# Kernel tuning notes

Hardware: AMD Instinct MI355X
Metric: run time of the kernel (lower is better)

The kernel has to match this reference:

```python
import jax, jax.numpy as jnp
import numpy as np

L = 8        # path length (number of visited nodes)
N = 32768    # neighbors per node (fixed fan-out)
H = 404      # relation_dim == GRU hidden size
D = 128      # node_encode_dim
F = 532      # neighbor feature = D + H
SCALE = 0.05


def setup_inputs() -> dict:
    key = jax.random.key(0)
    ks = jax.random.split(key, 14)
    return {
        "query": jax.random.normal(ks[0], (1, H), jnp.float32),
        "path_nodes": jax.random.normal(ks[1], (L, D), jnp.float32),
        "neighbors": jax.random.normal(ks[2], (L, N, F), jnp.float32),
        "action_ids": jax.random.randint(ks[3], (L - 1,), 0, N),
        "W_ih": jax.random.normal(ks[4], (3 * H, 3 * D), jnp.float32) * SCALE,
        "W_hh": jax.random.normal(ks[5], (3 * H, H), jnp.float32) * SCALE,
        "b_ih": jax.random.normal(ks[6], (3 * H,), jnp.float32) * SCALE,
        "b_hh": jax.random.normal(ks[7], (3 * H,), jnp.float32) * SCALE,
        "W_fa": jax.random.normal(ks[8], (D, F), jnp.float32) * SCALE,
        "b_fa": jax.random.normal(ks[9], (D,), jnp.float32) * SCALE,
        "W_fs": jax.random.normal(ks[10], (D, H), jnp.float32) * SCALE,
        "b_fs": jax.random.normal(ks[11], (D,), jnp.float32) * SCALE,
        "W_fp": jax.random.normal(ks[12], (1, 2 * D), jnp.float32) * SCALE,
        "b_fp": jax.random.normal(ks[13], (1,), jnp.float32) * SCALE,
    }


def gru_cell(x, h, W_ih, W_hh, b_ih, b_hh):
    # torch.nn.GRUCell semantics; x: (1, 3D), h: (1, H)
    gi = x @ W_ih.T + b_ih   # (1, 3H)
    gh = h @ W_hh.T + b_hh   # (1, 3H)
    i_r, i_z, i_n = jnp.split(gi, 3, axis=-1)
    h_r, h_z, h_n = jnp.split(gh, 3, axis=-1)
    r = jax.nn.sigmoid(i_r + h_r)
    z = jax.nn.sigmoid(i_z + h_z)
    n = jnp.tanh(i_n + r * h_n)
    return (1.0 - z) * n + z * h


def reference(query, path_nodes, neighbors, action_ids,
              W_ih, W_hh, b_ih, b_hh, W_fa, b_fa, W_fs, b_fs, W_fp, b_fp):
    # FA over all hops' neighbor blocks at once: (L, N, F) x (D, F) -> (L, N, D)
    hnts = jnp.einsum('lnf,df->lnd', neighbors, W_fa) + b_fa
    hmax = jnp.max(hnts, axis=1)                        # (L, D)  column-wise max (== _Max)
    hsel = hnts[jnp.arange(L - 1), action_ids]          # (L-1, D) chosen-action rows

    # initial GRU step: cat(zeros, zeros, first node emb) with query as hidden
    x0 = jnp.concatenate([jnp.zeros((1, 2 * D), query.dtype), path_nodes[0:1]], axis=1)
    qt = gru_cell(x0, query, W_ih, W_hh, b_ih, b_hh)

    def step(qt, inp):
        hAt, hat, nxt = inp                             # each (D,)
        x = jnp.concatenate([hAt, hat, nxt])[None, :]   # (1, 3D)
        return gru_cell(x, qt, W_ih, W_hh, b_ih, b_hh), None

    qt, _ = jax.lax.scan(step, qt, (hmax[:-1], hsel, path_nodes[1:]))

    hSt = qt @ W_fs.T + b_fs                            # (1, D)
    u0 = jnp.concatenate([hSt, hmax[-1:]], axis=1) @ W_fp.T + b_fp   # (1, 1)
    uks = hSt @ hnts[-1].T                              # (1, N)
    return jax.nn.softmax(jnp.concatenate([u0, uks], axis=1), axis=1)
```

## Files before the change

### kernel.cpp

```cpp
#include <hip/hip_runtime.h>
#include <math.h>

#define L 8
#define N 32768
#define H 404
#define D 128
#define F 532
#define KT 9
#define GRU_BLOCKS 101

typedef __attribute__((ext_vector_type(8))) _Float16 half8;
typedef __attribute__((ext_vector_type(4))) float f32x4;
typedef __attribute__((address_space(3))) unsigned int as3_u32;
typedef __attribute__((address_space(1))) unsigned int as1_u32;

#define WS_WH2     0
#define WS_HMAXK   (WS_WH2 + 36864)
#define WS_HSEL    (WS_HMAXK + L * D)
#define WS_GI      (WS_HSEL + (L - 1) * D)
#define WS_HBUF    (WS_GI + L * 3 * H)
#define WS_V       (WS_HBUF + 2 * H)
#define WS_HS      (WS_V + F)
#define WS_SCAL    (WS_HS + D)
#define WS_CNT     (WS_SCAL + 4)
#define WS_LOGITS  (WS_CNT + 4)

__device__ __forceinline__ unsigned encf(float f) {
    unsigned u = __float_as_uint(f);
    return (u & 0x80000000u) ? ~u : (u | 0x80000000u);
}
__device__ __forceinline__ float decf(unsigned u) {
    unsigned b = (u & 0x80000000u) ? (u ^ 0x80000000u) : ~u;
    return __uint_as_float(b);
}
__device__ __forceinline__ float sigmoidf_(float x) {
    return 1.0f / (1.0f + __expf(-x));
}
__device__ __forceinline__ unsigned pk_f16(float a, float b) {
    auto h = __builtin_amdgcn_cvt_pkrtz(a, b);
    return *(unsigned*)&h;
}
__device__ __forceinline__ half8 pack8(float4 x0, float4 x1) {
    uint4 u = { pk_f16(x0.x, x0.y), pk_f16(x0.z, x0.w),
                pk_f16(x1.x, x1.y), pk_f16(x1.z, x1.w) };
    return *(half8*)&u;
}
__device__ __forceinline__ void gld16(const void* g, void* l) {
    __builtin_amdgcn_global_load_lds((const as1_u32*)g, (as3_u32*)l, 16, 0, 0);
}

__global__ void k_prep(const float* __restrict__ Wfa, unsigned short* __restrict__ wh2,
                       unsigned* __restrict__ keys, unsigned* __restrict__ cnt) {
    int i = blockIdx.x * 256 + threadIdx.x;
    if (i < L * D) keys[i] = 0u;
    if (i == 2000) *cnt = 0u;
    if (i >= KT * 128 * 8) return;
    int kt = i / (128 * 8);
    int rem = i - kt * 128 * 8;
    int c = rem >> 3, j = rem & 7;
    int k0 = kt * 64 + (j ^ (c & 7)) * 8;
    unsigned short v[8];
#pragma unroll
    for (int e = 0; e < 8; ++e) {
        int k = k0 + e;
        float x = (k < F) ? Wfa[c * F + k] : 0.0f;
        _Float16 h = (_Float16)x;
        v[e] = *(unsigned short*)&h;
    }
    *(uint4*)(wh2 + (long)i * 8) = *(uint4*)v;
}

__global__ __launch_bounds__(256, 3)
void k_big(const float* __restrict__ nb, const unsigned short* __restrict__ wh2,
           const float* __restrict__ bfa, const int* __restrict__ aid,
           unsigned* __restrict__ hmaxk, float* __restrict__ hsel) {
    __shared__ float As[128 * 64];
    __shared__ unsigned short Bs[128 * 64];

    const int bid = blockIdx.x;
    const int l_hop = bid >> 8;
    const int row0 = (bid & 255) * 128;
    const int tid = threadIdx.x;
    const int lane = tid & 63, w = tid >> 6;
    const int wm = w >> 1, wn = w & 1;
    const int lr = lane & 15, kg = lane >> 4;

    const float* xbase = nb + ((long)l_hop * N + row0) * F;

    f32x4 acc[4][4];
    float bv[4];
#pragma unroll
    for (int n = 0; n < 4; ++n) bv[n] = bfa[wn * 64 + n * 16 + lr];
#pragma unroll
    for (int m = 0; m < 4; ++m)
#pragma unroll
        for (int n = 0; n < 4; ++n) {
            acc[m][n][0] = bv[n]; acc[m][n][1] = bv[n];
            acc[m][n][2] = bv[n]; acc[m][n][3] = bv[n];
        }

    const int srow = lane >> 4;
    const int scp  = lane & 15;

    for (int kt = 0; kt < KT; ++kt) {
        const int fc = kt * 64;
        __syncthreads();

#pragma unroll
        for (int it = 0; it < 8; ++it) {
            int rbase = it * 16 + w * 4;
            int row = rbase + srow;
            int cg = scp ^ (row & 7);
            int col0 = fc + cg * 4;
            const float* src = xbase + (long)row * F + ((col0 < F) ? col0 : 0);
            gld16(src, (char*)As + rbase * 256);
        }
#pragma unroll
        for (int it = 0; it < 4; ++it) {
            int rb = it * 32 + w * 8;
            const char* src = (const char*)wh2 + (long)kt * 16384 + rb * 128 + lane * 16;
            gld16(src, (char*)Bs + rb * 128);
        }
        __syncthreads();

#pragma unroll
        for (int ks = 0; ks < 2; ++ks) {
            half8 b[4];
#pragma unroll
            for (int n = 0; n < 4; ++n) {
                int col = wn * 64 + n * 16 + lr;
                int ch = (ks * 4 + kg) ^ (col & 7);
                b[n] = *(const half8*)((const char*)Bs + col * 128 + ch * 16);
            }
#pragma unroll
            for (int m = 0; m < 4; ++m) {
                int row = wm * 64 + m * 16 + lr;
                int c0 = ks * 8 + kg * 2;
                const char* base = (const char*)As + row * 256;
                float4 x0 = *(const float4*)(base + (((c0)     ^ (row & 7)) << 4));
                float4 x1 = *(const float4*)(base + (((c0 + 1) ^ (row & 7)) << 4));
                half8 a = pack8(x0, x1);
#pragma unroll
                for (int n = 0; n < 4; ++n)
                    acc[m][n] = __builtin_amdgcn_mfma_f32_16x16x32_f16(a, b[n], acc[m][n], 0, 0, 0);
            }
        }
    }

    __syncthreads();

    if (l_hop < L - 1) {
        int br = aid[l_hop] - row0;
        if (br >= 0 && br < 128 && (br >> 6) == wm && ((br >> 2) & 3) == kg) {
            int msel = (br >> 4) & 3, rsel = br & 3;
#pragma unroll
            for (int n = 0; n < 4; ++n) {
                float vsel = 0.f;
#pragma unroll
                for (int m = 0; m < 4; ++m)
#pragma unroll
                    for (int r = 0; r < 4; ++r)
                        if (m == msel && r == rsel) vsel = acc[m][n][r];
                hsel[l_hop * D + wn * 64 + n * 16 + lr] = vsel;
            }
        }
    }

    float cmax[4];
#pragma unroll
    for (int n = 0; n < 4; ++n) {
        float m0 = acc[0][n][0];
#pragma unroll
        for (int m = 0; m < 4; ++m)
#pragma unroll
            for (int r = 0; r < 4; ++r) m0 = fmaxf(m0, acc[m][n][r]);
        m0 = fmaxf(m0, __shfl_xor(m0, 16, 64));
        m0 = fmaxf(m0, __shfl_xor(m0, 32, 64));
        cmax[n] = m0;
    }
    float* wmaxp = (float*)As;
    if (kg == 0) {
#pragma unroll
        for (int n = 0; n < 4; ++n)
            wmaxp[wm * 128 + wn * 64 + n * 16 + lr] = cmax[n];
    }
    __syncthreads();
    if (tid < 128) {
        float mval = fmaxf(wmaxp[tid], wmaxp[128 + tid]);
        atomicMax(&hmaxk[l_hop * D + tid], encf(mval));
    }
}

__global__ void k_gi(const float* __restrict__ Wih, const float* __restrict__ bih,
                     const float* __restrict__ pn, const unsigned* __restrict__ hmaxk,
                     const float* __restrict__ hsel, float* __restrict__ gi) {
    __shared__ float xs[L][3 * D];
    const int tid = threadIdx.x;
    for (int i = tid; i < L * 3 * D; i += 256) {
        int t = i / (3 * D), k = i % (3 * D);
        float x;
        if (t == 0) {
            x = (k < 2 * D) ? 0.0f : pn[k - 2 * D];
        } else {
            if (k < D)            x = decf(hmaxk[(t - 1) * D + k]);
            else if (k < 2 * D)   x = hsel[(t - 1) * D + (k - D)];
            else                  x = pn[t * D + (k - 2 * D)];
        }
        xs[t][k] = x;
    }
    __syncthreads();

    const int lane = tid & 63;
    const int row = blockIdx.x * 4 + (tid >> 6);
    const float* wr = Wih + (long)row * 3 * D;
    float s[L];
#pragma unroll
    for (int t = 0; t < L; ++t) s[t] = 0.f;
#pragma unroll
    for (int c = 0; c < 6; ++c) {
        int k = lane + c * 64;
        float wv = wr[k];
#pragma unroll
        for (int t = 0; t < L; ++t) s[t] = fmaf(wv, xs[t][k], s[t]);
    }
#pragma unroll
    for (int t = 0; t < L; ++t)
        for (int off = 1; off < 64; off <<= 1) s[t] += __shfl_xor(s[t], off, 64);
    if (lane == 0) {
        float b = bih[row];
#pragma unroll
        for (int t = 0; t < L; ++t) gi[t * 3 * H + row] = s[t] + b;
    }
}

__global__ __launch_bounds__(256, 1)
void k_gru(const float* __restrict__ Whh, const float* __restrict__ bhh,
           const float* __restrict__ gi, const float* __restrict__ query,
           float* __restrict__ hbuf, unsigned* __restrict__ cnt) {
    const int tid = threadIdx.x;
    const int lane = tid & 63;
    const int j = blockIdx.x * 4 + (tid >> 6);

    float wr[7], wz[7], wnn[7];
#pragma unroll
    for (int c = 0; c < 7; ++c) {
        int i = lane + c * 64;
        bool ok = i < H;
        wr[c]  = ok ? Whh[(long)j * H + i]           : 0.f;
        wz[c]  = ok ? Whh[(long)(H + j) * H + i]     : 0.f;
        wnn[c] = ok ? Whh[(long)(2 * H + j) * H + i] : 0.f;
    }
    float b_r = 0.f, b_z = 0.f, b_n = 0.f;
    if (lane == 0) { b_r = bhh[j]; b_z = bhh[H + j]; b_n = bhh[2 * H + j]; }

    for (int t = 0; t < L; ++t) {
        const float* hin = (t == 0) ? query : (hbuf + ((t - 1) & 1) * H);
        float* hout = hbuf + (t & 1) * H;
        float pr = 0.f, pz = 0.f, pn2 = 0.f;
#pragma unroll
        for (int c = 0; c < 7; ++c) {
            int i = lane + c * 64;
            float hv = 0.f;
            if (i < H)
                hv = (t == 0) ? hin[i]
                              : __hip_atomic_load(hin + i, __ATOMIC_RELAXED,
                                                  __HIP_MEMORY_SCOPE_AGENT);
            pr  = fmaf(wr[c],  hv, pr);
            pz  = fmaf(wz[c],  hv, pz);
            pn2 = fmaf(wnn[c], hv, pn2);
        }
        for (int off = 1; off < 64; off <<= 1) {
            pr  += __shfl_xor(pr, off, 64);
            pz  += __shfl_xor(pz, off, 64);
            pn2 += __shfl_xor(pn2, off, 64);
        }
        if (lane == 0) {
            const float* gt = gi + t * 3 * H;
            float hprev = (t == 0) ? hin[j]
                                   : __hip_atomic_load(hin + j, __ATOMIC_RELAXED,
                                                       __HIP_MEMORY_SCOPE_AGENT);
            float r  = sigmoidf_(gt[j] + pr + b_r);
            float z  = sigmoidf_(gt[H + j] + pz + b_z);
            float nn = tanhf(gt[2 * H + j] + r * (pn2 + b_n));
            float hv = (1.0f - z) * nn + z * hprev;
            __hip_atomic_store(hout + j, hv, __ATOMIC_RELAXED,
                               __HIP_MEMORY_SCOPE_AGENT);
        }
        if (t < L - 1) {
            __syncthreads();
            if (tid == 0) {
                __hip_atomic_fetch_add(cnt, 1u, __ATOMIC_RELEASE,
                                       __HIP_MEMORY_SCOPE_AGENT);
                unsigned target = (unsigned)GRU_BLOCKS * (t + 1);
                while (__hip_atomic_load(cnt, __ATOMIC_ACQUIRE,
                                         __HIP_MEMORY_SCOPE_AGENT) < target)
                    __builtin_amdgcn_s_sleep(2);
            }
            __syncthreads();
        }
    }
}

__global__ void k_final(const float* __restrict__ qt, const float* __restrict__ Wfs,
                        const float* __restrict__ bfs, const float* __restrict__ Wfp,
                        const float* __restrict__ bfp, const float* __restrict__ bfa,
                        const float* __restrict__ Wfa, const unsigned* __restrict__ hmaxk,
                        float* __restrict__ v, float* __restrict__ scal,
                        float* __restrict__ logits) {
    __shared__ float hs[D];
    int tid = threadIdx.x, lane = tid & 63, wid = tid >> 6;
#pragma unroll
    for (int dd = 0; dd < 8; ++dd) {
        int d = wid * 8 + dd;
        float s = 0.f;
#pragma unroll
        for (int c = 0; c < 7; ++c) {
            int i = lane + c * 64;
            if (i < H) s = fmaf(qt[i], Wfs[(long)d * H + i], s);
        }
        for (int off = 1; off < 64; off <<= 1) s += __shfl_xor(s, off, 64);
        if (lane == 0) hs[d] = s + bfs[d];
    }
    __syncthreads();
    if (tid < F) {
        float s = 0.f;
#pragma unroll 16
        for (int d = 0; d < D; ++d) s = fmaf(hs[d], Wfa[(long)d * F + tid], s);
        v[tid] = s;
    } else if (tid == F) {
        float s = bfp[0];
        for (int d = 0; d < D; ++d) {
            s = fmaf(hs[d], Wfp[d], s);
            s = fmaf(decf(hmaxk[(L - 1) * D + d]), Wfp[D + d], s);
        }
        logits[0] = s;
    } else if (tid == F + 1) {
        float c2 = 0.f;
        for (int d = 0; d < D; ++d) c2 = fmaf(hs[d], bfa[d], c2);
        scal[0] = c2;
    }
}

__global__ void k_uks(const float* __restrict__ nb7, const float* __restrict__ v,
                      const float* __restrict__ scal, float* __restrict__ logits) {
    long n = (long)blockIdx.x * 4 + (threadIdx.x >> 6);
    int lane = threadIdx.x & 63;
    const float* row = nb7 + n * F;
    float s = 0.f;
    for (int f = lane; f < F; f += 64) s = fmaf(v[f], row[f], s);
    for (int off = 1; off < 64; off <<= 1) s += __shfl_xor(s, off, 64);
    if (lane == 0) logits[1 + n] = s + scal[0];
}

__global__ void k_sm12(const float* __restrict__ logits, float* __restrict__ scal) {
    __shared__ float sm[16], ss[16];
    int tid = threadIdx.x, lane = tid & 63, wid = tid >> 6;
    float m = -3.4e38f, s = 0.f;
    for (int i = tid; i <= N; i += 1024) {
        float x = logits[i];
        if (x > m) { s = s * __expf(m - x) + 1.0f; m = x; }
        else       { s += __expf(x - m); }
    }
    for (int off = 1; off < 64; off <<= 1) {
        float m2 = __shfl_xor(m, off, 64);
        float s2 = __shfl_xor(s, off, 64);
        float M = fmaxf(m, m2);
        s = s * __expf(m - M) + s2 * __expf(m2 - M);
        m = M;
    }
    if (lane == 0) { sm[wid] = m; ss[wid] = s; }
    __syncthreads();
    if (tid == 0) {
        float M = sm[0], S = 0.f;
        for (int k = 1; k < 16; ++k) M = fmaxf(M, sm[k]);
        for (int k = 0; k < 16; ++k) S += ss[k] * __expf(sm[k] - M);
        scal[1] = M; scal[2] = S;
    }
}

__global__ void k_sm3(const float* __restrict__ logits, const float* __restrict__ scal,
                      float* __restrict__ out) {
    int i = blockIdx.x * 256 + threadIdx.x;
    if (i <= N) out[i] = __expf(logits[i] - scal[1]) / scal[2];
}

extern "C" void kernel_launch(void* const* d_in, const int* in_sizes, int n_in,
                              void* d_out, int out_size, void* d_ws, size_t ws_size,
                              hipStream_t stream) {
    const float* query = (const float*)d_in[0];
    const float* pn    = (const float*)d_in[1];
    const float* nb    = (const float*)d_in[2];
    const int*   aid   = (const int*)d_in[3];
    const float* Wih   = (const float*)d_in[4];
    const float* Whh   = (const float*)d_in[5];
    const float* bih   = (const float*)d_in[6];
    const float* bhh   = (const float*)d_in[7];
    const float* Wfa   = (const float*)d_in[8];
    const float* bfa   = (const float*)d_in[9];
    const float* Wfs   = (const float*)d_in[10];
    const float* bfs   = (const float*)d_in[11];
    const float* Wfp   = (const float*)d_in[12];
    const float* bfp   = (const float*)d_in[13];

    float* ws = (float*)d_ws;
    unsigned short* wh2   = (unsigned short*)(ws + WS_WH2);
    unsigned*       hmaxk = (unsigned*)(ws + WS_HMAXK);
    unsigned*       cnt   = (unsigned*)(ws + WS_CNT);
    float* hsel   = ws + WS_HSEL;
    float* gi     = ws + WS_GI;
    float* hbuf   = ws + WS_HBUF;
    float* v      = ws + WS_V;
    float* scal   = ws + WS_SCAL;
    float* logits = ws + WS_LOGITS;
    float* out    = (float*)d_out;

    k_prep<<<(KT * 128 * 8 + 255) / 256, 256, 0, stream>>>(Wfa, wh2, hmaxk, cnt);
    k_big <<<L * 256, 256, 0, stream>>>(nb, wh2, bfa, aid, hmaxk, hsel);
    k_gi  <<<303, 256, 0, stream>>>(Wih, bih, pn, hmaxk, hsel, gi);
    k_gru <<<GRU_BLOCKS, 256, 0, stream>>>(Whh, bhh, gi, query, hbuf, cnt);

    const float* qt = hbuf + ((L - 1) & 1) * H;
    k_final<<<1, 1024, 0, stream>>>(qt, Wfs, bfs, Wfp, bfp, bfa, Wfa, hmaxk, v, scal, logits);
    k_uks  <<<N / 4, 256, 0, stream>>>(nb + (long)(L - 1) * N * F, v, scal, logits);

    k_sm12<<<1, 1024, 0, stream>>>(logits, scal);
    k_sm3 <<<(N + 1 + 255) / 256, 256, 0, stream>>>(logits, scal, out);
}
```

Baseline: 226.0 us.

## Double-buffer k_big LDS tiles with 32-wide K steps and async prefetch

The big FA GEMM kernel moves from single-buffered 64-wide K tiles to double-buffered 32-wide K tiles. The next-next tile's global-to-LDS loads are issued while the current tile computes, with explicit vmcnt waits and barriers replacing the full syncthreads pairs. The fp16 weight pre-pack is reorganised into a K-group-major layout to match the new tile shape. This is meant to hide global load latency behind MFMA work. In exchange it adds more barriers per K element and depends on hand-tuned waitcnt values.

```diff
diff --git a/kernel.cpp b/kernel.cpp
--- a/kernel.cpp
+++ b/kernel.cpp
@@ -6,7 +6,7 @@
 #define H 404
 #define D 128
 #define F 532
-#define KT 9
+#define NT 17
 #define GRU_BLOCKS 101
 
 typedef __attribute__((ext_vector_type(8))) _Float16 half8;
@@ -54,11 +54,11 @@
     int i = blockIdx.x * 256 + threadIdx.x;
     if (i < L * D) keys[i] = 0u;
     if (i == 2000) *cnt = 0u;
-    if (i >= KT * 128 * 8) return;
-    int kt = i / (128 * 8);
-    int rem = i - kt * 128 * 8;
-    int c = rem >> 3, j = rem & 7;
-    int k0 = kt * 64 + (j ^ (c & 7)) * 8;
+    if (i >= NT * 4 * 128) return;
+    int tile = i >> 9;
+    int rem = i & 511;
+    int kg = rem >> 7, c = rem & 127;
+    int k0 = tile * 32 + kg * 8;
     unsigned short v[8];
 #pragma unroll
     for (int e = 0; e < 8; ++e) {
@@ -74,8 +74,8 @@
 void k_big(const float* __restrict__ nb, const unsigned short* __restrict__ wh2,
            const float* __restrict__ bfa, const int* __restrict__ aid,
            unsigned* __restrict__ hmaxk, float* __restrict__ hsel) {
-    __shared__ float As[128 * 64];
-    __shared__ unsigned short Bs[128 * 64];
+    __shared__ float As[2][128 * 32];
+    __shared__ unsigned short Bs[2][128 * 32];
 
     const int bid = blockIdx.x;
     const int l_hop = bid >> 8;
@@ -99,53 +99,65 @@
             acc[m][n][2] = bv[n]; acc[m][n][3] = bv[n];
         }
 
-    const int srow = lane >> 4;
-    const int scp  = lane & 15;
-
-    for (int kt = 0; kt < KT; ++kt) {
-        const int fc = kt * 64;
-        __syncthreads();
-
-#pragma unroll
-        for (int it = 0; it < 8; ++it) {
-            int rbase = it * 16 + w * 4;
-            int row = rbase + srow;
-            int cg = scp ^ (row & 7);
+    const int srw = lane >> 3;
+    const int sch = lane & 7;
+
+    auto STAGE = [&](int kt, int buf) {
+        const int fc = kt * 32;
+#pragma unroll
+        for (int it = 0; it < 4; ++it) {
+            int rbase = it * 32 + w * 8;
+            int row = rbase + srw;
+            int cg = sch ^ srw;
             int col0 = fc + cg * 4;
             const float* src = xbase + (long)row * F + ((col0 < F) ? col0 : 0);
-            gld16(src, (char*)As + rbase * 256);
-        }
-#pragma unroll
-        for (int it = 0; it < 4; ++it) {
-            int rb = it * 32 + w * 8;
-            const char* src = (const char*)wh2 + (long)kt * 16384 + rb * 128 + lane * 16;
-            gld16(src, (char*)Bs + rb * 128);
-        }
-        __syncthreads();
-
-#pragma unroll
-        for (int ks = 0; ks < 2; ++ks) {
-            half8 b[4];
-#pragma unroll
-            for (int n = 0; n < 4; ++n) {
-                int col = wn * 64 + n * 16 + lr;
-                int ch = (ks * 4 + kg) ^ (col & 7);
-                b[n] = *(const half8*)((const char*)Bs + col * 128 + ch * 16);
-            }
-#pragma unroll
-            for (int m = 0; m < 4; ++m) {
-                int row = wm * 64 + m * 16 + lr;
-                int c0 = ks * 8 + kg * 2;
-                const char* base = (const char*)As + row * 256;
-                float4 x0 = *(const float4*)(base + (((c0)     ^ (row & 7)) << 4));
-                float4 x1 = *(const float4*)(base + (((c0 + 1) ^ (row & 7)) << 4));
-                half8 a = pack8(x0, x1);
-#pragma unroll
-                for (int n = 0; n < 4; ++n)
-                    acc[m][n] = __builtin_amdgcn_mfma_f32_16x16x32_f16(a, b[n], acc[m][n], 0, 0, 0);
-            }
-        }
-    }
+            gld16(src, (char*)As[buf] + rbase * 128);
+        }
+#pragma unroll
+        for (int it = 0; it < 2; ++it) {
+            int off = it * 4096 + w * 1024;
+            gld16((const char*)wh2 + (long)kt * 8192 + off + lane * 16,
+                  (char*)Bs[buf] + off);
+        }
+    };
+
+    auto CMP = [&](int buf) {
+        const char* Ab = (const char*)As[buf];
+        const char* Bb = (const char*)Bs[buf];
+        half8 b[4];
+#pragma unroll
+        for (int n = 0; n < 4; ++n)
+            b[n] = *(const half8*)(Bb + kg * 2048 + (wn * 64 + n * 16 + lr) * 16);
+#pragma unroll
+        for (int m = 0; m < 4; ++m) {
+            int row = wm * 64 + m * 16 + lr;
+            const char* base = Ab + row * 128;
+            int c0 = kg * 2;
+            float4 x0 = *(const float4*)(base + ((c0 ^ (row & 7)) << 4));
+            float4 x1 = *(const float4*)(base + (((c0 + 1) ^ (row & 7)) << 4));
+            half8 a = pack8(x0, x1);
+#pragma unroll
+            for (int n = 0; n < 4; ++n)
+                acc[m][n] = __builtin_amdgcn_mfma_f32_16x16x32_f16(a, b[n], acc[m][n], 0, 0, 0);
+        }
+    };
+
+    STAGE(0, 0);
+    STAGE(1, 1);
+
+    for (int kt = 0; kt < NT - 1; ++kt) {
+        asm volatile("s_waitcnt vmcnt(6)" ::: "memory");
+        __builtin_amdgcn_s_barrier();
+        __builtin_amdgcn_sched_barrier(0);
+        CMP(kt & 1);
+        __builtin_amdgcn_s_barrier();
+        __builtin_amdgcn_sched_barrier(0);
+        if (kt + 2 < NT) STAGE(kt + 2, kt & 1);
+    }
+    asm volatile("s_waitcnt vmcnt(0)" ::: "memory");
+    __builtin_amdgcn_s_barrier();
+    __builtin_amdgcn_sched_barrier(0);
+    CMP((NT - 1) & 1);
 
     __syncthreads();
 
@@ -414,7 +426,7 @@
     float* logits = ws + WS_LOGITS;
     float* out    = (float*)d_out;
 
-    k_prep<<<(KT * 128 * 8 + 255) / 256, 256, 0, stream>>>(Wfa, wh2, hmaxk, cnt);
+    k_prep<<<(NT * 4 * 128 + 255) / 256, 256, 0, stream>>>(Wfa, wh2, hmaxk, cnt);
     k_big <<<L * 256, 256, 0, stream>>>(nb, wh2, bfa, aid, hmaxk, hsel);
     k_gi  <<<303, 256, 0, stream>>>(Wih, bih, pn, hmaxk, hsel, gi);
     k_gru <<<GRU_BLOCKS, 256, 0, stream>>>(Whh, bhh, gi, query, hbuf, cnt);
```

Measured after the change: 233.6 us. 1.03x slower.

## Store last-hop FA outputs and fuse GRU, final, and softmax stages with grid barriers

Applied to the files above, without the earlier changes.

k_big now writes the last hop's projected hnts rows (N×D) to workspace, so the final logits become a D-length dot per row instead of re-reading the F-wide neighbor block. The input projection, GRU recurrence, hSt projection and u0 are fused into one persistent kernel with software grid barriers. The logits, the online softmax reduction and the normalization are fused into a second kernel with grid barriers. This removes several launches and a re-read of the last neighbor slab. The cost is an extra N×D store, and the design relies on all 1024 or 303 blocks being co-resident for the spin barriers to avoid deadlock.

```diff
diff --git a/kernel.cpp b/kernel.cpp
--- a/kernel.cpp
+++ b/kernel.cpp
@@ -7,7 +7,7 @@
 #define D 128
 #define F 532
 #define KT 9
-#define GRU_BLOCKS 101
+#define GRU_BLK 101
 
 typedef __attribute__((ext_vector_type(8))) _Float16 half8;
 typedef __attribute__((ext_vector_type(4))) float f32x4;
@@ -15,15 +15,17 @@
 typedef __attribute__((address_space(1))) unsigned int as1_u32;
 
 #define WS_WH2     0
-#define WS_HMAXK   (WS_WH2 + 36864)
-#define WS_HSEL    (WS_HMAXK + L * D)
-#define WS_GI      (WS_HSEL + (L - 1) * D)
-#define WS_HBUF    (WS_GI + L * 3 * H)
-#define WS_V       (WS_HBUF + 2 * H)
-#define WS_HS      (WS_V + F)
-#define WS_SCAL    (WS_HS + D)
-#define WS_CNT     (WS_SCAL + 4)
-#define WS_LOGITS  (WS_CNT + 4)
+#define WS_HMAXK   36864
+#define WS_HSEL    37888
+#define WS_GI      38784
+#define WS_HBUF    48480
+#define WS_HS      49288
+#define WS_SCAL    49416
+#define WS_CNT     49420
+#define WS_PM      49424
+#define WS_PS      50448
+#define WS_LOGITS  51472
+#define WS_HNTS7   84992
 
 __device__ __forceinline__ unsigned encf(float f) {
     unsigned u = __float_as_uint(f);
@@ -48,12 +50,27 @@
 __device__ __forceinline__ void gld16(const void* g, void* l) {
     __builtin_amdgcn_global_load_lds((const as1_u32*)g, (as3_u32*)l, 16, 0, 0);
 }
+__device__ __forceinline__ float aload(const float* p) {
+    return __hip_atomic_load(p, __ATOMIC_RELAXED, __HIP_MEMORY_SCOPE_AGENT);
+}
+__device__ __forceinline__ void astore(float* p, float v) {
+    __hip_atomic_store(p, v, __ATOMIC_RELAXED, __HIP_MEMORY_SCOPE_AGENT);
+}
+__device__ __forceinline__ void gbar(unsigned* cnt, unsigned target) {
+    __syncthreads();
+    if (threadIdx.x == 0) {
+        __hip_atomic_fetch_add(cnt, 1u, __ATOMIC_RELEASE, __HIP_MEMORY_SCOPE_AGENT);
+        while (__hip_atomic_load(cnt, __ATOMIC_ACQUIRE, __HIP_MEMORY_SCOPE_AGENT) < target)
+            __builtin_amdgcn_s_sleep(2);
+    }
+    __syncthreads();
+}
 
 __global__ void k_prep(const float* __restrict__ Wfa, unsigned short* __restrict__ wh2,
-                       unsigned* __restrict__ keys, unsigned* __restrict__ cnt) {
+                       unsigned* __restrict__ keys, unsigned* __restrict__ cnts) {
     int i = blockIdx.x * 256 + threadIdx.x;
     if (i < L * D) keys[i] = 0u;
-    if (i == 2000) *cnt = 0u;
+    if (i >= 2000 && i < 2003) cnts[i - 2000] = 0u;
     if (i >= KT * 128 * 8) return;
     int kt = i / (128 * 8);
     int rem = i - kt * 128 * 8;
@@ -73,7 +90,8 @@
 __global__ __launch_bounds__(256, 3)
 void k_big(const float* __restrict__ nb, const unsigned short* __restrict__ wh2,
            const float* __restrict__ bfa, const int* __restrict__ aid,
-           unsigned* __restrict__ hmaxk, float* __restrict__ hsel) {
+           unsigned* __restrict__ hmaxk, float* __restrict__ hsel,
+           float* __restrict__ hnts7) {
     __shared__ float As[128 * 64];
     __shared__ unsigned short Bs[128 * 64];
 
@@ -105,7 +123,6 @@
     for (int kt = 0; kt < KT; ++kt) {
         const int fc = kt * 64;
         __syncthreads();
-
 #pragma unroll
         for (int it = 0; it < 8; ++it) {
             int rbase = it * 16 + w * 4;
@@ -164,6 +181,19 @@
                 hsel[l_hop * D + wn * 64 + n * 16 + lr] = vsel;
             }
         }
+    } else {
+        float* hbase = hnts7 + (long)row0 * D;
+#pragma unroll
+        for (int m = 0; m < 4; ++m) {
+            int rb = wm * 64 + m * 16 + kg * 4;
+#pragma unroll
+            for (int r = 0; r < 4; ++r) {
+                float* rowp = hbase + (long)(rb + r) * D + wn * 64 + lr;
+#pragma unroll
+                for (int n = 0; n < 4; ++n)
+                    rowp[n * 16] = acc[m][n][r];
+            }
+        }
     }
 
     float cmax[4];
@@ -191,11 +221,23 @@
     }
 }
 
-__global__ void k_gi(const float* __restrict__ Wih, const float* __restrict__ bih,
-                     const float* __restrict__ pn, const unsigned* __restrict__ hmaxk,
-                     const float* __restrict__ hsel, float* __restrict__ gi) {
+__global__ __launch_bounds__(256)
+void k_fuseA(const float* __restrict__ Wih, const float* __restrict__ bih,
+             const float* __restrict__ pn, const unsigned* __restrict__ hmaxk,
+             const float* __restrict__ hsel, const float* __restrict__ Whh,
+             const float* __restrict__ bhh, const float* __restrict__ query,
+             const float* __restrict__ Wfs, const float* __restrict__ bfs,
+             const float* __restrict__ Wfp, const float* __restrict__ bfp,
+             float* __restrict__ gi, float* __restrict__ hbuf,
+             float* __restrict__ hs_ws, float* __restrict__ logits,
+             unsigned* __restrict__ cnts) {
     __shared__ float xs[L][3 * D];
+    const int bid = blockIdx.x;
     const int tid = threadIdx.x;
+    const int lane = tid & 63, w4 = tid >> 6;
+    unsigned* cntA = cnts + 0;
+    unsigned* cntG = cnts + 1;
+
     for (int i = tid; i < L * 3 * D; i += 256) {
         int t = i / (3 * D), k = i % (3 * D);
         float x;
@@ -209,179 +251,201 @@
         xs[t][k] = x;
     }
     __syncthreads();
-
-    const int lane = tid & 63;
-    const int row = blockIdx.x * 4 + (tid >> 6);
-    const float* wr = Wih + (long)row * 3 * D;
-    float s[L];
-#pragma unroll
-    for (int t = 0; t < L; ++t) s[t] = 0.f;
-#pragma unroll
-    for (int c = 0; c < 6; ++c) {
-        int k = lane + c * 64;
-        float wv = wr[k];
-#pragma unroll
-        for (int t = 0; t < L; ++t) s[t] = fmaf(wv, xs[t][k], s[t]);
-    }
-#pragma unroll
-    for (int t = 0; t < L; ++t)
-        for (int off = 1; off < 64; off <<= 1) s[t] += __shfl_xor(s[t], off, 64);
-    if (lane == 0) {
-        float b = bih[row];
-#pragma unroll
-        for (int t = 0; t < L; ++t) gi[t * 3 * H + row] = s[t] + b;
-    }
-}
-
-__global__ __launch_bounds__(256, 1)
-void k_gru(const float* __restrict__ Whh, const float* __restrict__ bhh,
-           const float* __restrict__ gi, const float* __restrict__ query,
-           float* __restrict__ hbuf, unsigned* __restrict__ cnt) {
-    const int tid = threadIdx.x;
-    const int lane = tid & 63;
-    const int j = blockIdx.x * 4 + (tid >> 6);
-
-    float wr[7], wz[7], wnn[7];
-#pragma unroll
-    for (int c = 0; c < 7; ++c) {
-        int i = lane + c * 64;
-        bool ok = i < H;
-        wr[c]  = ok ? Whh[(long)j * H + i]           : 0.f;
-        wz[c]  = ok ? Whh[(long)(H + j) * H + i]     : 0.f;
-        wnn[c] = ok ? Whh[(long)(2 * H + j) * H + i] : 0.f;
-    }
-    float b_r = 0.f, b_z = 0.f, b_n = 0.f;
-    if (lane == 0) { b_r = bhh[j]; b_z = bhh[H + j]; b_n = bhh[2 * H + j]; }
-
-    for (int t = 0; t < L; ++t) {
-        const float* hin = (t == 0) ? query : (hbuf + ((t - 1) & 1) * H);
-        float* hout = hbuf + (t & 1) * H;
-        float pr = 0.f, pz = 0.f, pn2 = 0.f;
+    {
+        const int row = bid * 4 + w4;
+        const float* wr = Wih + (long)row * 3 * D;
+        float s[L];
+#pragma unroll
+        for (int t = 0; t < L; ++t) s[t] = 0.f;
+#pragma unroll
+        for (int c = 0; c < 6; ++c) {
+            int k = lane + c * 64;
+            float wv = wr[k];
+#pragma unroll
+            for (int t = 0; t < L; ++t) s[t] = fmaf(wv, xs[t][k], s[t]);
+        }
+#pragma unroll
+        for (int t = 0; t < L; ++t)
+            for (int off = 1; off < 64; off <<= 1) s[t] += __shfl_xor(s[t], off, 64);
+        if (lane == 0) {
+            float b = bih[row];
+#pragma unroll
+            for (int t = 0; t < L; ++t) astore(&gi[t * 3 * H + row], s[t] + b);
+        }
+    }
+    gbar(cntA, 303);
+
+    if (bid < GRU_BLK) {
+        const int j = bid * 4 + w4;
+        float wr[7], wz[7], wnn[7];
 #pragma unroll
         for (int c = 0; c < 7; ++c) {
             int i = lane + c * 64;
-            float hv = 0.f;
-            if (i < H)
-                hv = (t == 0) ? hin[i]
-                              : __hip_atomic_load(hin + i, __ATOMIC_RELAXED,
-                                                  __HIP_MEMORY_SCOPE_AGENT);
-            pr  = fmaf(wr[c],  hv, pr);
-            pz  = fmaf(wz[c],  hv, pz);
-            pn2 = fmaf(wnn[c], hv, pn2);
-        }
-        for (int off = 1; off < 64; off <<= 1) {
-            pr  += __shfl_xor(pr, off, 64);
-            pz  += __shfl_xor(pz, off, 64);
-            pn2 += __shfl_xor(pn2, off, 64);
-        }
-        if (lane == 0) {
-            const float* gt = gi + t * 3 * H;
-            float hprev = (t == 0) ? hin[j]
-                                   : __hip_atomic_load(hin + j, __ATOMIC_RELAXED,
-                                                       __HIP_MEMORY_SCOPE_AGENT);
-            float r  = sigmoidf_(gt[j] + pr + b_r);
-            float z  = sigmoidf_(gt[H + j] + pz + b_z);
-            float nn = tanhf(gt[2 * H + j] + r * (pn2 + b_n));
-            float hv = (1.0f - z) * nn + z * hprev;
-            __hip_atomic_store(hout + j, hv, __ATOMIC_RELAXED,
-                               __HIP_MEMORY_SCOPE_AGENT);
-        }
-        if (t < L - 1) {
-            __syncthreads();
-            if (tid == 0) {
-                __hip_atomic_fetch_add(cnt, 1u, __ATOMIC_RELEASE,
-                                       __HIP_MEMORY_SCOPE_AGENT);
-                unsigned target = (unsigned)GRU_BLOCKS * (t + 1);
-                while (__hip_atomic_load(cnt, __ATOMIC_ACQUIRE,
-                                         __HIP_MEMORY_SCOPE_AGENT) < target)
-                    __builtin_amdgcn_s_sleep(2);
-            }
-            __syncthreads();
-        }
-    }
-}
-
-__global__ void k_final(const float* __restrict__ qt, const float* __restrict__ Wfs,
-                        const float* __restrict__ bfs, const float* __restrict__ Wfp,
-                        const float* __restrict__ bfp, const float* __restrict__ bfa,
-                        const float* __restrict__ Wfa, const unsigned* __restrict__ hmaxk,
-                        float* __restrict__ v, float* __restrict__ scal,
-                        float* __restrict__ logits) {
-    __shared__ float hs[D];
-    int tid = threadIdx.x, lane = tid & 63, wid = tid >> 6;
-#pragma unroll
-    for (int dd = 0; dd < 8; ++dd) {
-        int d = wid * 8 + dd;
+            bool ok = i < H;
+            wr[c]  = ok ? Whh[(long)j * H + i]           : 0.f;
+            wz[c]  = ok ? Whh[(long)(H + j) * H + i]     : 0.f;
+            wnn[c] = ok ? Whh[(long)(2 * H + j) * H + i] : 0.f;
+        }
+        float b_r = 0.f, b_z = 0.f, b_n = 0.f;
+        if (lane == 0) { b_r = bhh[j]; b_z = bhh[H + j]; b_n = bhh[2 * H + j]; }
+
+        for (int t = 0; t < L; ++t) {
+            const float* hin = (t == 0) ? query : (hbuf + ((t - 1) & 1) * H);
+            float* hout = hbuf + (t & 1) * H;
+            float pr = 0.f, pz = 0.f, pn2 = 0.f;
+#pragma unroll
+            for (int c = 0; c < 7; ++c) {
+                int i = lane + c * 64;
+                float hv = 0.f;
+                if (i < H) hv = (t == 0) ? hin[i] : aload(hin + i);
+                pr  = fmaf(wr[c],  hv, pr);
+                pz  = fmaf(wz[c],  hv, pz);
+                pn2 = fmaf(wnn[c], hv, pn2);
+            }
+            for (int off = 1; off < 64; off <<= 1) {
+                pr  += __shfl_xor(pr, off, 64);
+                pz  += __shfl_xor(pz, off, 64);
+                pn2 += __shfl_xor(pn2, off, 64);
+            }
+            if (lane == 0) {
+                float g0 = aload(&gi[t * 3 * H + j]);
+                float g1 = aload(&gi[t * 3 * H + H + j]);
+                float g2 = aload(&gi[t * 3 * H + 2 * H + j]);
+                float hprev = (t == 0) ? hin[j] : aload(hin + j);
+                float r  = sigmoidf_(g0 + pr + b_r);
+                float z  = sigmoidf_(g1 + pz + b_z);
+                float nn = tanhf(g2 + r * (pn2 + b_n));
+                astore(hout + j, (1.0f - z) * nn + z * hprev);
+            }
+            if (t < L - 1) {
+                __syncthreads();
+                if (tid == 0) {
+                    __hip_atomic_fetch_add(cntG, 1u, __ATOMIC_RELEASE,
+                                           __HIP_MEMORY_SCOPE_AGENT);
+                    unsigned target = (unsigned)GRU_BLK * (t + 1);
+                    while (__hip_atomic_load(cntG, __ATOMIC_ACQUIRE,
+                                             __HIP_MEMORY_SCOPE_AGENT) < target)
+                        __builtin_amdgcn_s_sleep(2);
+                }
+                __syncthreads();
+            }
+        }
+    }
+    gbar(cntA, 2 * 303);
+
+    if (bid < 32) {
+        const float* qt = hbuf + H;
+        int d = bid * 4 + w4;
         float s = 0.f;
 #pragma unroll
         for (int c = 0; c < 7; ++c) {
             int i = lane + c * 64;
-            if (i < H) s = fmaf(qt[i], Wfs[(long)d * H + i], s);
+            if (i < H) s = fmaf(aload(qt + i), Wfs[(long)d * H + i], s);
         }
         for (int off = 1; off < 64; off <<= 1) s += __shfl_xor(s, off, 64);
-        if (lane == 0) hs[d] = s + bfs[d];
-    }
-    __syncthreads();
-    if (tid < F) {
-        float s = 0.f;
-#pragma unroll 16
-        for (int d = 0; d < D; ++d) s = fmaf(hs[d], Wfa[(long)d * F + tid], s);
-        v[tid] = s;
-    } else if (tid == F) {
-        float s = bfp[0];
-        for (int d = 0; d < D; ++d) {
-            s = fmaf(hs[d], Wfp[d], s);
-            s = fmaf(decf(hmaxk[(L - 1) * D + d]), Wfp[D + d], s);
-        }
-        logits[0] = s;
-    } else if (tid == F + 1) {
-        float c2 = 0.f;
-        for (int d = 0; d < D; ++d) c2 = fmaf(hs[d], bfa[d], c2);
-        scal[0] = c2;
-    }
-}
-
-__global__ void k_uks(const float* __restrict__ nb7, const float* __restrict__ v,
-                      const float* __restrict__ scal, float* __restrict__ logits) {
-    long n = (long)blockIdx.x * 4 + (threadIdx.x >> 6);
-    int lane = threadIdx.x & 63;
-    const float* row = nb7 + n * F;
-    float s = 0.f;
-    for (int f = lane; f < F; f += 64) s = fmaf(v[f], row[f], s);
-    for (int off = 1; off < 64; off <<= 1) s += __shfl_xor(s, off, 64);
-    if (lane == 0) logits[1 + n] = s + scal[0];
-}
-
-__global__ void k_sm12(const float* __restrict__ logits, float* __restrict__ scal) {
-    __shared__ float sm[16], ss[16];
-    int tid = threadIdx.x, lane = tid & 63, wid = tid >> 6;
-    float m = -3.4e38f, s = 0.f;
-    for (int i = tid; i <= N; i += 1024) {
-        float x = logits[i];
-        if (x > m) { s = s * __expf(m - x) + 1.0f; m = x; }
-        else       { s += __expf(x - m); }
-    }
-    for (int off = 1; off < 64; off <<= 1) {
-        float m2 = __shfl_xor(m, off, 64);
-        float s2 = __shfl_xor(s, off, 64);
-        float M = fmaxf(m, m2);
-        s = s * __expf(m - M) + s2 * __expf(m2 - M);
-        m = M;
-    }
-    if (lane == 0) { sm[wid] = m; ss[wid] = s; }
-    __syncthreads();
-    if (tid == 0) {
-        float M = sm[0], S = 0.f;
-        for (int k = 1; k < 16; ++k) M = fmaxf(M, sm[k]);
-        for (int k = 0; k < 16; ++k) S += ss[k] * __expf(sm[k] - M);
-        scal[1] = M; scal[2] = S;
-    }
-}
-
-__global__ void k_sm3(const float* __restrict__ logits, const float* __restrict__ scal,
-                      float* __restrict__ out) {
-    int i = blockIdx.x * 256 + threadIdx.x;
-    if (i <= N) out[i] = __expf(logits[i] - scal[1]) / scal[2];
+        if (lane == 0) astore(&hs_ws[d], s + bfs[d]);
+    }
+    gbar(cntA, 3 * 303);
+
+    if (bid == 0 && w4 == 0) {
+        float s = fmaf(aload(&hs_ws[lane]),      Wfp[lane],       0.f);
+        s = fmaf(aload(&hs_ws[lane + 64]),       Wfp[lane + 64],  s);
+        s = fmaf(decf(hmaxk[(L - 1) * D + lane]),      Wfp[D + lane],      s);
+        s = fmaf(decf(hmaxk[(L - 1) * D + lane + 64]), Wfp[D + lane + 64], s);
+        for (int off = 1; off < 64; off <<= 1) s += __shfl_xor(s, off, 64);
+        if (lane == 0) astore(&logits[0], s + bfp[0]);
+    }
+}
+
+__global__ __launch_bounds__(256)
+void k_fuseB(const float* __restrict__ hnts7, const float* __restrict__ hs_ws,
+             float* __restrict__ logits, float* __restrict__ pm,
+             float* __restrict__ ps, float* __restrict__ scal,
+             float* __restrict__ out, unsigned* __restrict__ cnts) {
+    __shared__ float wpm[4], wps[4], rm[4], rs[4];
+    const int bid = blockIdx.x;
+    const int tid = threadIdx.x;
+    const int lane = tid & 63, w4 = tid >> 6;
+    unsigned* cntB = cnts + 2;
+
+    {
+        float h0 = hs_ws[lane * 2];
+        float h1 = hs_ws[lane * 2 + 1];
+        float mw = -3.4e38f, sw = 0.f;
+#pragma unroll
+        for (int r = 0; r < 8; ++r) {
+            int n = bid * 32 + w4 * 8 + r;
+            float2 x = *(const float2*)(hnts7 + (long)n * D + lane * 2);
+            float s = h0 * x.x + h1 * x.y;
+            for (int off = 1; off < 64; off <<= 1) s += __shfl_xor(s, off, 64);
+            if (lane == 0) {
+                astore(&logits[1 + n], s);
+                if (s > mw) { sw = sw * __expf(mw - s) + 1.0f; mw = s; }
+                else        { sw += __expf(s - mw); }
+            }
+        }
+        if (lane == 0) { wpm[w4] = mw; wps[w4] = sw; }
+        __syncthreads();
+        if (tid == 0) {
+            float M = -3.4e38f, S = 0.f;
+#pragma unroll
+            for (int k = 0; k < 4; ++k) {
+                float Mn = fmaxf(M, wpm[k]);
+                S = S * __expf(M - Mn) + wps[k] * __expf(wpm[k] - Mn);
+                M = Mn;
+            }
+            if (bid == 0) {
+                float t0 = logits[0];
+                float Mn = fmaxf(M, t0);
+                S = S * __expf(M - Mn) + __expf(t0 - Mn);
+                M = Mn;
+            }
+            astore(&pm[bid], M); astore(&ps[bid], S);
+        }
+    }
+    gbar(cntB, 1024);
+
+    if (bid == 0) {
+        float M = -3.4e38f, S = 0.f;
+#pragma unroll
+        for (int k = 0; k < 4; ++k) {
+            int i = tid * 4 + k;
+            float m2 = aload(&pm[i]), s2 = aload(&ps[i]);
+            float Mn = fmaxf(M, m2);
+            S = S * __expf(M - Mn) + s2 * __expf(m2 - Mn);
+            M = Mn;
+        }
+        for (int off = 1; off < 64; off <<= 1) {
+            float m2 = __shfl_xor(M, off, 64);
+            float s2 = __shfl_xor(S, off, 64);
+            float Mn = fmaxf(M, m2);
+            S = S * __expf(M - Mn) + s2 * __expf(m2 - Mn);
+            M = Mn;
+        }
+        if (lane == 0) { rm[w4] = M; rs[w4] = S; }
+        __syncthreads();
+        if (tid == 0) {
+            float Mf = -3.4e38f, Sf = 0.f;
+#pragma unroll
+            for (int k = 0; k < 4; ++k) {
+                float Mn = fmaxf(Mf, rm[k]);
+                Sf = Sf * __expf(Mf - Mn) + rs[k] * __expf(rm[k] - Mn);
+                Mf = Mn;
+            }
+            astore(&scal[1], Mf); astore(&scal[2], Sf);
+        }
+    }
+    gbar(cntB, 2048);
+
+    {
+        float M = aload(&scal[1]), S = aload(&scal[2]);
+        if (tid < 32) {
+            int n = bid * 32 + tid;
+            out[1 + n] = __expf(aload(&logits[1 + n]) - M) / S;
+        }
+        if (bid == 0 && tid == 32)
+            out[0] = __expf(logits[0] - M) / S;
+    }
 }
 
 extern "C" void kernel_launch(void* const* d_in, const int* in_sizes, int n_in,
@@ -405,24 +469,21 @@
     float* ws = (float*)d_ws;
     unsigned short* wh2   = (unsigned short*)(ws + WS_WH2);
     unsigned*       hmaxk = (unsigned*)(ws + WS_HMAXK);
-    unsigned*       cnt   = (unsigned*)(ws + WS_CNT);
+    unsigned*       cnts  = (unsigned*)(ws + WS_CNT);
     float* hsel   = ws + WS_HSEL;
     float* gi     = ws + WS_GI;
     float* hbuf   = ws + WS_HBUF;
-    float* v      = ws + WS_V;
+    float* hs_ws  = ws + WS_HS;
     float* scal   = ws + WS_SCAL;
+    float* pm     = ws + WS_PM;
+    float* psum   = ws + WS_PS;
     float* logits = ws + WS_LOGITS;
+    float* hnts7  = ws + WS_HNTS7;
     float* out    = (float*)d_out;
 
-    k_prep<<<(KT * 128 * 8 + 255) / 256, 256, 0, stream>>>(Wfa, wh2, hmaxk, cnt);
-    k_big <<<L * 256, 256, 0, stream>>>(nb, wh2, bfa, aid, hmaxk, hsel);
-    k_gi  <<<303, 256, 0, stream>>>(Wih, bih, pn, hmaxk, hsel, gi);
-    k_gru <<<GRU_BLOCKS, 256, 0, stream>>>(Whh, bhh, gi, query, hbuf, cnt);
-
-    const float* qt = hbuf + ((L - 1) & 1) * H;
-    k_final<<<1, 1024, 0, stream>>>(qt, Wfs, bfs, Wfp, bfp, bfa, Wfa, hmaxk, v, scal, logits);
-    k_uks  <<<N / 4, 256, 0, stream>>>(nb + (long)(L - 1) * N * F, v, scal, logits);
-
-    k_sm12<<<1, 1024, 0, stream>>>(logits, scal);
-    k_sm3 <<<(N + 1 + 255) / 256, 256, 0, stream>>>(logits, scal, out);
-}
+    k_prep <<<(KT * 128 * 8 + 255) / 256, 256, 0, stream>>>(Wfa, wh2, hmaxk, cnts);
+    k_big  <<<L * 256, 256, 0, stream>>>(nb, wh2, bfa, aid, hmaxk, hsel, hnts7);
+    k_fuseA<<<303, 256, 0, stream>>>(Wih, bih, pn, hmaxk, hsel, Whh, bhh, query,
+                                     Wfs, bfs, Wfp, bfp, gi, hbuf, hs_ws, logits, cnts);
+    k_fuseB<<<1024, 256, 0, stream>>>(hnts7, hs_ws, logits, pm, psum, scal, out, cnts);
+}
```

Measured after the change: 478.8 us. 2.12x slower.

## Read FA weight fragments directly from global memory, drop LDS staging of B

Applied to the files above, without the earlier changes.

The prep kernel now lays out the fp16 W_fa tile in MFMA-fragment order, so each lane's half8 B operand is one contiguous 16-byte global load. k_big no longer stages B through shared memory, which halves its LDS footprint and lets launch bounds rise to 4 blocks per SM. The cost is that every block re-reads the B fragments from global memory or cache on each K step instead of once per tile into LDS, which adds load latency inside the MFMA loop.

```diff
diff --git a/kernel.cpp b/kernel.cpp
--- a/kernel.cpp
+++ b/kernel.cpp
@@ -14,8 +14,8 @@
 typedef __attribute__((address_space(3))) unsigned int as3_u32;
 typedef __attribute__((address_space(1))) unsigned int as1_u32;
 
-#define WS_WH2     0
-#define WS_HMAXK   (WS_WH2 + 36864)
+#define WS_WH3     0
+#define WS_HMAXK   (WS_WH3 + 36864)
 #define WS_HSEL    (WS_HMAXK + L * D)
 #define WS_GI      (WS_HSEL + (L - 1) * D)
 #define WS_HBUF    (WS_GI + L * 3 * H)
@@ -49,33 +49,32 @@
     __builtin_amdgcn_global_load_lds((const as1_u32*)g, (as3_u32*)l, 16, 0, 0);
 }
 
-__global__ void k_prep(const float* __restrict__ Wfa, unsigned short* __restrict__ wh2,
+__global__ void k_prep(const float* __restrict__ Wfa, unsigned short* __restrict__ wh3,
                        unsigned* __restrict__ keys, unsigned* __restrict__ cnt) {
     int i = blockIdx.x * 256 + threadIdx.x;
     if (i < L * D) keys[i] = 0u;
     if (i == 2000) *cnt = 0u;
-    if (i >= KT * 128 * 8) return;
-    int kt = i / (128 * 8);
-    int rem = i - kt * 128 * 8;
-    int c = rem >> 3, j = rem & 7;
-    int k0 = kt * 64 + (j ^ (c & 7)) * 8;
+    if (i >= KT * 8 * 128) return;
+    int kt = i >> 10;
+    int rem = i & 1023;
+    int c8 = rem >> 7, col = rem & 127;
+    int k0 = kt * 64 + c8 * 8;
     unsigned short v[8];
 #pragma unroll
     for (int e = 0; e < 8; ++e) {
         int k = k0 + e;
-        float x = (k < F) ? Wfa[c * F + k] : 0.0f;
+        float x = (k < F) ? Wfa[col * F + k] : 0.0f;
         _Float16 h = (_Float16)x;
         v[e] = *(unsigned short*)&h;
     }
-    *(uint4*)(wh2 + (long)i * 8) = *(uint4*)v;
-}
-
-__global__ __launch_bounds__(256, 3)
-void k_big(const float* __restrict__ nb, const unsigned short* __restrict__ wh2,
+    *(uint4*)(wh3 + (long)i * 8) = *(uint4*)v;
+}
+
+__global__ __launch_bounds__(256, 4)
+void k_big(const float* __restrict__ nb, const unsigned short* __restrict__ wh3,
            const float* __restrict__ bfa, const int* __restrict__ aid,
            unsigned* __restrict__ hmaxk, float* __restrict__ hsel) {
     __shared__ float As[128 * 64];
-    __shared__ unsigned short Bs[128 * 64];
 
     const int bid = blockIdx.x;
     const int l_hop = bid >> 8;
@@ -115,12 +114,6 @@
             const float* src = xbase + (long)row * F + ((col0 < F) ? col0 : 0);
             gld16(src, (char*)As + rbase * 256);
         }
-#pragma unroll
-        for (int it = 0; it < 4; ++it) {
-            int rb = it * 32 + w * 8;
-            const char* src = (const char*)wh2 + (long)kt * 16384 + rb * 128 + lane * 16;
-            gld16(src, (char*)Bs + rb * 128);
-        }
         __syncthreads();
 
 #pragma unroll
@@ -128,9 +121,8 @@
             half8 b[4];
 #pragma unroll
             for (int n = 0; n < 4; ++n) {
-                int col = wn * 64 + n * 16 + lr;
-                int ch = (ks * 4 + kg) ^ (col & 7);
-                b[n] = *(const half8*)((const char*)Bs + col * 128 + ch * 16);
+                long bo = (((long)kt * 8 + ks * 4 + kg) * 128 + wn * 64 + n * 16 + lr) * 8;
+                b[n] = *(const half8*)(wh3 + bo);
             }
 #pragma unroll
             for (int m = 0; m < 4; ++m) {
@@ -403,7 +395,7 @@
     const float* bfp   = (const float*)d_in[13];
 
     float* ws = (float*)d_ws;
-    unsigned short* wh2   = (unsigned short*)(ws + WS_WH2);
+    unsigned short* wh3   = (unsigned short*)(ws + WS_WH3);
     unsigned*       hmaxk = (unsigned*)(ws + WS_HMAXK);
     unsigned*       cnt   = (unsigned*)(ws + WS_CNT);
     float* hsel   = ws + WS_HSEL;
@@ -414,8 +406,8 @@
     float* logits = ws + WS_LOGITS;
     float* out    = (float*)d_out;
 
-    k_prep<<<(KT * 128 * 8 + 255) / 256, 256, 0, stream>>>(Wfa, wh2, hmaxk, cnt);
-    k_big <<<L * 256, 256, 0, stream>>>(nb, wh2, bfa, aid, hmaxk, hsel);
+    k_prep<<<(KT * 8 * 128 + 255) / 256, 256, 0, stream>>>(Wfa, wh3, hmaxk, cnt);
+    k_big <<<L * 256, 256, 0, stream>>>(nb, wh3, bfa, aid, hmaxk, hsel);
     k_gi  <<<303, 256, 0, stream>>>(Wih, bih, pn, hmaxk, hsel, gi);
     k_gru <<<GRU_BLOCKS, 256, 0, stream>>>(Whh, bhh, gi, query, hbuf, cnt);
 
```

After: 283.7 us. 1.25x slower.
